# Performance work log

Measured on AMD Instinct MI355X. Metric: run time of the kernel, lower is better.

Reference implementation:

```python
import jax, jax.numpy as jnp
import numpy as np

LN_EPS = 1e-12


def setup_inputs() -> dict:
    key = jax.random.key(0)
    ks = jax.random.split(key, 10)
    B, S, W, D, H = 16, 512, 5, 200, 768
    std = 0.02
    return {
        "layer_output": jax.random.normal(ks[0], (B, S, H), dtype=jnp.float32),
        "word_embeddings": jax.random.normal(ks[1], (B, S, W, D), dtype=jnp.float32),
        "word_mask": jax.random.randint(ks[2], (B, S, W), 0, 2, dtype=jnp.int64),
        "W1": jax.random.normal(ks[3], (D, H), dtype=jnp.float32) * std,
        "b1": jnp.zeros((H,), dtype=jnp.float32),
        "W2": jax.random.normal(ks[4], (H, H), dtype=jnp.float32) * std,
        "b2": jnp.zeros((H,), dtype=jnp.float32),
        "attn_W": jax.random.normal(ks[5], (H, H), dtype=jnp.float32) * std,
        "ln_gamma": jnp.ones((H,), dtype=jnp.float32),
        "ln_beta": jnp.zeros((H,), dtype=jnp.float32),
    }


def reference(layer_output, word_embeddings, word_mask, W1, b1, W2, b2, attn_W, ln_gamma, ln_beta):
    # word_transform: Linear -> Tanh -> Linear (dropout = identity in eval)
    we = jnp.tanh(jnp.einsum("bswd,dh->bswh", word_embeddings, W1) + b1)
    we = jnp.einsum("bswh,hk->bswk", we, W2) + b2  # [B,S,W,H]

    # bilinear word attention: (x @ attn_W) . word_outputs -> score over W
    q = jnp.einsum("bsh,hk->bsk", layer_output, attn_W)  # [B,S,H]
    alpha = jnp.einsum("bsk,bswk->bsw", q, we)            # [B,S,W]
    alpha = alpha + (1.0 - word_mask.astype(alpha.dtype)) * -10000.0
    alpha = jax.nn.softmax(alpha, axis=-1)

    # weighted sum over words + residual
    agg = jnp.einsum("bsw,bswh->bsh", alpha, we)
    h = layer_output + agg

    # LayerNorm (fuse_layer; dropout = identity in eval)
    mu = jnp.mean(h, axis=-1, keepdims=True)
    var = jnp.mean(jnp.square(h - mu), axis=-1, keepdims=True)
    return (h - mu) * jax.lax.rsqrt(var + LN_EPS) * ln_gamma + ln_beta
```

## Files before the change

### kernel.cpp

```cpp
#include <hip/hip_runtime.h>
#include <hip/hip_bf16.h>
#include <math.h>


typedef __attribute__((ext_vector_type(8))) short bf16x8;
typedef __attribute__((ext_vector_type(4))) float f32x4;

__device__ __forceinline__ unsigned short f2bf_bits(float f) {
    __hip_bfloat16 h = __float2bfloat16(f);
    return *reinterpret_cast<unsigned short*>(&h);
}
__device__ __forceinline__ float bf_bits2f(unsigned short u) {
    union { unsigned int i; float f; } v; v.i = ((unsigned int)u) << 16; return v.f;
}
__device__ __forceinline__ float tanh_fast(float x) {
    float xc = fminf(fmaxf(x, -9.f), 9.f);
    float t  = __expf(2.f * xc);
    return (t - 1.f) * __builtin_amdgcn_rcpf(t + 1.f);
}

__device__ __forceinline__ void async_cp16(const void* g, void* lds) {
#if __has_builtin(__builtin_amdgcn_global_load_lds)
    auto gp = (const __attribute__((address_space(1))) unsigned int*)g;
    auto lp = (__attribute__((address_space(3))) unsigned int*)lds;
    __builtin_amdgcn_global_load_lds(gp, lp, 16, 0, 0);
#else
    *(uint4*)lds = *(const uint4*)g;
#endif
}

__device__ __forceinline__ void sched_fence()  { asm volatile("" ::: "memory"); }
__device__ __forceinline__ void wait8_barrier(){ asm volatile("s_waitcnt vmcnt(8)\ns_barrier" ::: "memory"); }
__device__ __forceinline__ void wait0_barrier(){ asm volatile("s_waitcnt vmcnt(0)\ns_barrier" ::: "memory"); }
__device__ __forceinline__ void barrier_only() { asm volatile("s_barrier" ::: "memory"); }

template<bool HAS_BIAS, bool TANH_ACT, bool RESID, bool OUT_BF16, int N, int K, int KREAL>
__device__ __forceinline__ void gemm_body(
    const __hip_bfloat16* __restrict__ A,
    const __hip_bfloat16* __restrict__ Bt,
    const float* __restrict__ bias,
    const float* __restrict__ resid,
    void* __restrict__ outp,
    int m0, int n0, unsigned char* smem)
{
    constexpr int NIT = K / 64;

    const int tid  = threadIdx.x;
    const int lane = tid & 63;
    const int wave = tid >> 6;
    const int wm   = wave & 1;
    const int wn   = wave >> 1;

    const int rsub = lane >> 3;
    const int slot = lane & 7;
    const int kc   = slot ^ rsub;
    const __hip_bfloat16* gA = A  + (size_t)(m0 + wave * 32 + rsub) * K + kc * 8;
    const __hip_bfloat16* gB = Bt + (size_t)(n0 + wave * 32 + rsub) * K + kc * 8;
    unsigned short* lA0 = (unsigned short*)smem + wave * 2048 + lane * 8;
    unsigned short* lB0 = lA0 + 8192;

    const int row16 = lane & 15;
    const int kq    = lane >> 4;

    f32x4 acc[4][4];
#pragma unroll
    for (int i = 0; i < 4; i++)
#pragma unroll
        for (int j = 0; j < 4; j++) acc[i][j] = (f32x4){0.f, 0.f, 0.f, 0.f};

    auto stage = [&](int t) {
        unsigned short* lA = lA0 + (t & 1) * 16384;
        unsigned short* lB = lB0 + (t & 1) * 16384;
        const __hip_bfloat16* a = gA + t * 64;
        const __hip_bfloat16* b = gB + t * 64;
#pragma unroll
        for (int i = 0; i < 4; i++) {
            async_cp16(a + (size_t)(8 * i) * K, lA + i * 512);
            async_cp16(b + (size_t)(8 * i) * K, lB + i * 512);
        }
        sched_fence();
    };

    stage(0);
    if (NIT > 1) stage(1);

#pragma unroll
    for (int t = 0; t < NIT; ++t) {
        if (t == NIT - 1) wait0_barrier(); else wait8_barrier();

        const unsigned short* As = (const unsigned short*)(smem + (t & 1) * 32768);
        const unsigned short* Bs = As + 8192;
        const bool full = (t * 64 + 32 < KREAL);

        bf16x8 af[2][4], bg[2][4];
#pragma unroll
        for (int mi = 0; mi < 4; mi++) {
            const int r = wm * 64 + mi * 16 + row16;
            af[0][mi] = *(const bf16x8*)&As[r * 64 + (kq ^ (r & 7)) * 8];
            if (full) af[1][mi] = *(const bf16x8*)&As[r * 64 + ((4 + kq) ^ (r & 7)) * 8];
        }
#pragma unroll
        for (int ni = 0; ni < 4; ni++) {
            const int r = wn * 64 + ni * 16 + row16;
            bg[0][ni] = *(const bf16x8*)&Bs[r * 64 + (kq ^ (r & 7)) * 8];
            if (full) bg[1][ni] = *(const bf16x8*)&Bs[r * 64 + ((4 + kq) ^ (r & 7)) * 8];
        }
#pragma unroll
        for (int mi = 0; mi < 4; mi++)
#pragma unroll
            for (int ni = 0; ni < 4; ni++)
                acc[mi][ni] = __builtin_amdgcn_mfma_f32_16x16x32_bf16(
                    af[0][mi], bg[0][ni], acc[mi][ni], 0, 0, 0);
        if (full) {
#pragma unroll
            for (int mi = 0; mi < 4; mi++)
#pragma unroll
                for (int ni = 0; ni < 4; ni++)
                    acc[mi][ni] = __builtin_amdgcn_mfma_f32_16x16x32_bf16(
                        af[1][mi], bg[1][ni], acc[mi][ni], 0, 0, 0);
        }
        barrier_only();
        if (t + 2 < NIT) stage(t + 2);
    }

    if (OUT_BF16) {
        unsigned short* rep = (unsigned short*)smem;
#pragma unroll
        for (int ni = 0; ni < 4; ni++) {
            const int c = wn * 64 + ni * 16 + row16;
            float bcol = HAS_BIAS ? bias[n0 + c] : 0.f;
#pragma unroll
            for (int mi = 0; mi < 4; mi++)
#pragma unroll
                for (int r = 0; r < 4; r++) {
                    const int rr = wm * 64 + mi * 16 + kq * 4 + r;
                    float v = acc[mi][ni][r];
                    if (HAS_BIAS) v += bcol;
                    if (TANH_ACT) v = tanh_fast(v);
                    rep[rr * 132 + c] = f2bf_bits(v);
                }
        }
        __syncthreads();
#pragma unroll
        for (int p = 0; p < 8; p++) {
            const int lin = p * 256 + tid;
            const int row = lin >> 4;
            const int c8  = lin & 15;
            const unsigned short* s = &rep[row * 132 + c8 * 8];
            union { uint4 u; unsigned long long q[2]; } d;
            d.q[0] = *(const unsigned long long*)(s);
            d.q[1] = *(const unsigned long long*)(s + 4);
            *(uint4*)((__hip_bfloat16*)outp + (size_t)(m0 + row) * N + n0 + c8 * 8) = d.u;
        }
    } else {
        float* rep = (float*)smem;
#pragma unroll
        for (int h = 0; h < 2; h++) {
            if (wm == h) {
#pragma unroll
                for (int ni = 0; ni < 4; ni++) {
                    const int c = wn * 64 + ni * 16 + row16;
                    float bcol = HAS_BIAS ? bias[n0 + c] : 0.f;
#pragma unroll
                    for (int mi = 0; mi < 4; mi++)
#pragma unroll
                        for (int r = 0; r < 4; r++) {
                            const int rr = mi * 16 + kq * 4 + r;
                            float v = acc[mi][ni][r];
                            if (HAS_BIAS) v += bcol;
                            if (TANH_ACT) v = tanh_fast(v);
                            rep[rr * 132 + c] = v;
                        }
                }
            }
            __syncthreads();
#pragma unroll
            for (int p = 0; p < 8; p++) {
                const int lin = p * 256 + tid;
                const int row = lin >> 5;
                const int c4  = lin & 31;
                float4 v = *(const float4*)&rep[row * 132 + c4 * 4];
                const int grow = m0 + h * 64 + row;
                if (RESID) {
                    float4 rv = *(const float4*)&resid[(size_t)grow * N + n0 + c4 * 4];
                    v.x += rv.x; v.y += rv.y; v.z += rv.z; v.w += rv.w;
                }
                *(float4*)((float*)outp + (size_t)grow * N + n0 + c4 * 4) = v;
            }
            __syncthreads();
        }
    }
}

template<bool HAS_BIAS, bool TANH_ACT, bool RESID, bool OUT_BF16, int N, int K, int GX>
__global__ __launch_bounds__(256) void mfma_gemm(
    const __hip_bfloat16* __restrict__ A,
    const __hip_bfloat16* __restrict__ Bt,
    const float* __restrict__ bias,
    const float* __restrict__ resid,
    void* __restrict__ outp)
{
    __shared__ __align__(16) unsigned char smem[65536];
    int bx, by;
    {
        const int total = gridDim.x;
        const int per_xcd = total >> 3;
        if ((total & 7) == 0 && (per_xcd % GX) == 0) {
            int xcd = blockIdx.x & 7, idx = blockIdx.x >> 3;
            int lin = xcd * per_xcd + idx;
            by = lin / GX; bx = lin % GX;
        } else { by = blockIdx.x / GX; bx = blockIdx.x % GX; }
    }
    gemm_body<HAS_BIAS, TANH_ACT, RESID, OUT_BF16, N, K, K>(
        A, Bt, bias, resid, outp, by * 128, bx * 128, smem);
}

__global__ __launch_bounds__(256) void tct_kernel(
    const __hip_bfloat16* __restrict__ Eb,   const __hip_bfloat16* __restrict__ W1Tb,
    const float* __restrict__ b1,            __hip_bfloat16* __restrict__ Tb,
    const __hip_bfloat16* __restrict__ W2b,  const __hip_bfloat16* __restrict__ attnb,
    __hip_bfloat16* __restrict__ Ctb)
{
    __shared__ __align__(16) unsigned char smem[65536];
    if (blockIdx.x < 36) {
        const int id = blockIdx.x;
        gemm_body<false, false, false, true, 768, 768, 768>(
            W2b, attnb, nullptr, nullptr, Ctb, (id / 6) * 128, (id % 6) * 128, smem);
    } else {
        const int idq = blockIdx.x - 36;
        const int xcd = idq & 7, idx = idq >> 3;
        const int lin = xcd * 240 + idx;
        gemm_body<true, true, false, true, 768, 256, 224>(
            Eb, W1Tb, b1, nullptr, Tb, (lin / 6) * 128, (lin % 6) * 128, smem);
    }
}

__global__ __launch_bounds__(256) void prep_kernel(
    const float* __restrict__ x,  __hip_bfloat16* __restrict__ xb,
    const float* __restrict__ w2, __hip_bfloat16* __restrict__ w2b,
    const float* __restrict__ aw, __hip_bfloat16* __restrict__ awb,
    const float* __restrict__ E,  __hip_bfloat16* __restrict__ Eb,
    const float* __restrict__ W1, __hip_bfloat16* __restrict__ W1Tb,
    __hip_bfloat16* __restrict__ W2Tb)
{
    __shared__ float tile[32][33];
    const int b = blockIdx.x, tid = threadIdx.x;
    if (b < 6144 + 576 + 576) {
        const float* src; __hip_bfloat16* dst; long long i;
        if (b < 6144)      { src = x;  dst = xb;  i = (long long)b * 256 + tid; }
        else if (b < 6720) { src = w2; dst = w2b; i = (long long)(b - 6144) * 256 + tid; }
        else               { src = aw; dst = awb; i = (long long)(b - 6720) * 256 + tid; }
        float4 v = ((const float4*)src)[i];
        ((ushort4*)dst)[i] = make_ushort4(f2bf_bits(v.x), f2bf_bits(v.y), f2bf_bits(v.z), f2bf_bits(v.w));
    } else if (b < 7296 + 10240) {
        const int lane = tid & 63, wave = tid >> 6;
        const long long row = (long long)(b - 7296) * 4 + wave;
        const int k = lane * 4;
        float4 v = make_float4(0.f, 0.f, 0.f, 0.f);
        if (k < 200) v = *(const float4*)&E[row * 200 + k];
        *(ushort4*)&Eb[row * 256 + k] =
            make_ushort4(f2bf_bits(v.x), f2bf_bits(v.y), f2bf_bits(v.z), f2bf_bits(v.w));
    } else {
        const float* in; __hip_bfloat16* outb; int R, C, Rpad, t;
        if (b < 17536 + 192) { t = b - 17536; in = W1; outb = W1Tb; R = 200; C = 768; Rpad = 256; }
        else                 { t = b - 17728; in = w2; outb = W2Tb; R = 768; C = 768; Rpad = 768; }
        const int c0 = (t % 24) * 32, r0 = (t / 24) * 32;
        const int xx = tid & 31, yy = tid >> 5;
#pragma unroll
        for (int i = 0; i < 32; i += 8) {
            int r = r0 + yy + i;
            tile[yy + i][xx] = (r < R) ? in[(size_t)r * C + c0 + xx] : 0.f;
        }
        __syncthreads();
#pragma unroll
        for (int i = 0; i < 32; i += 8)
            outb[(size_t)(c0 + yy + i) * Rpad + r0 + xx] = __float2bfloat16(tile[xx][yy + i]);
    }
}

__global__ __launch_bounds__(256) void attn_kernel(
    const __hip_bfloat16* __restrict__ T,
    const __hip_bfloat16* P,
    const int* __restrict__ mask,
    __hip_bfloat16* S)
{
    const int lane = threadIdx.x & 63;
    const int wave = threadIdx.x >> 6;
    const int r    = blockIdx.x * 4 + wave;
    const int base = lane * 12;

    float pv[12];
    {
        const ushort4* pp = (const ushort4*)((const unsigned short*)P + (size_t)r * 768 + base);
        ushort4 u0 = pp[0], u1 = pp[1], u2 = pp[2];
        unsigned short us[12] = {u0.x,u0.y,u0.z,u0.w, u1.x,u1.y,u1.z,u1.w, u2.x,u2.y,u2.z,u2.w};
#pragma unroll
        for (int j = 0; j < 12; j++) pv[j] = bf_bits2f(us[j]);
    }
    float tv[5][12], part[5];
#pragma unroll
    for (int w = 0; w < 5; w++) {
        const ushort4* tp = (const ushort4*)((const unsigned short*)T + ((size_t)r * 5 + w) * 768 + base);
        ushort4 u0 = tp[0], u1 = tp[1], u2 = tp[2];
        unsigned short us[12] = {u0.x,u0.y,u0.z,u0.w, u1.x,u1.y,u1.z,u1.w, u2.x,u2.y,u2.z,u2.w};
        float s = 0.f;
#pragma unroll
        for (int j = 0; j < 12; j++) { tv[w][j] = bf_bits2f(us[j]); s += tv[w][j] * pv[j]; }
        part[w] = s;
    }
#pragma unroll
    for (int off = 32; off > 0; off >>= 1)
#pragma unroll
        for (int w = 0; w < 5; w++)
            part[w] += __shfl_xor(part[w], off, 64);

    float logit[5], mx = -1e30f;
#pragma unroll
    for (int w = 0; w < 5; w++) {
        float m = (float)mask[(size_t)r * 5 + w];
        logit[w] = part[w] - 10000.0f * (1.0f - m);
        mx = fmaxf(mx, logit[w]);
    }
    float se = 0.f;
#pragma unroll
    for (int w = 0; w < 5; w++) { logit[w] = expf(logit[w] - mx); se += logit[w]; }
    const float inv = 1.0f / se;

    unsigned short os[12];
#pragma unroll
    for (int j = 0; j < 12; j++) {
        float s = 0.f;
#pragma unroll
        for (int w = 0; w < 5; w++) s += logit[w] * tv[w][j];
        os[j] = f2bf_bits(s * inv);
    }
    ushort4* sp = (ushort4*)((unsigned short*)S + (size_t)r * 768 + base);
    sp[0] = make_ushort4(os[0], os[1], os[2],  os[3]);
    sp[1] = make_ushort4(os[4], os[5], os[6],  os[7]);
    sp[2] = make_ushort4(os[8], os[9], os[10], os[11]);
}

__global__ __launch_bounds__(256) void ln_kernel(
    const float* __restrict__ Hbuf, const float* __restrict__ gamma,
    const float* __restrict__ beta, float* __restrict__ out)
{
    const int lane = threadIdx.x & 63;
    const int wave = threadIdx.x >> 6;
    const int r    = blockIdx.x * 4 + wave;
    const float* hr = Hbuf + (size_t)r * 768 + lane * 12;

    float v[12];
    {
        float4 a = *(const float4*)(hr);
        float4 b = *(const float4*)(hr + 4);
        float4 c = *(const float4*)(hr + 8);
        v[0]=a.x; v[1]=a.y; v[2]=a.z; v[3]=a.w;
        v[4]=b.x; v[5]=b.y; v[6]=b.z; v[7]=b.w;
        v[8]=c.x; v[9]=c.y; v[10]=c.z; v[11]=c.w;
    }
    float s = 0.f;
#pragma unroll
    for (int j = 0; j < 12; j++) s += v[j];
#pragma unroll
    for (int off = 32; off > 0; off >>= 1) s += __shfl_xor(s, off, 64);
    const float mu = s * (1.f / 768.f);
    float vs = 0.f;
#pragma unroll
    for (int j = 0; j < 12; j++) { float d = v[j] - mu; vs += d * d; }
#pragma unroll
    for (int off = 32; off > 0; off >>= 1) vs += __shfl_xor(vs, off, 64);
    const float rs = rsqrtf(vs * (1.f / 768.f) + 1e-12f);

    float o[12];
#pragma unroll
    for (int j = 0; j < 12; j++) {
        int h = lane * 12 + j;
        o[j] = (v[j] - mu) * rs * gamma[h] + beta[h];
    }
    float* orow = out + (size_t)r * 768 + lane * 12;
    *(float4*)(orow)     = make_float4(o[0], o[1], o[2],  o[3]);
    *(float4*)(orow + 4) = make_float4(o[4], o[5], o[6],  o[7]);
    *(float4*)(orow + 8) = make_float4(o[8], o[9], o[10], o[11]);
}

extern "C" void kernel_launch(void* const* d_in, const int* in_sizes, int n_in,
                              void* d_out, int out_size, void* d_ws, size_t ws_size,
                              hipStream_t stream)
{
    const float* x      = (const float*)d_in[0];
    const float* E      = (const float*)d_in[1];
    const int*   mask   = (const int*)d_in[2];
    const float* W1     = (const float*)d_in[3];
    const float* b1     = (const float*)d_in[4];
    const float* W2     = (const float*)d_in[5];
    const float* b2     = (const float*)d_in[6];
    const float* attn_W = (const float*)d_in[7];
    const float* gamma  = (const float*)d_in[8];
    const float* beta   = (const float*)d_in[9];
    float* out = (float*)d_out;

    const int BS = 8192, H = 768, M1 = 40960, KP = 256;

    char* p = (char*)d_ws;
    auto alloc = [&](size_t bytes) { char* q = p; p += (bytes + 255) & ~(size_t)255; return q; };
    __hip_bfloat16* xb    = (__hip_bfloat16*)alloc((size_t)BS * H * 2);
    __hip_bfloat16* W2b   = (__hip_bfloat16*)alloc((size_t)H * H * 2);
    __hip_bfloat16* W2Tb  = (__hip_bfloat16*)alloc((size_t)H * H * 2);
    __hip_bfloat16* attnb = (__hip_bfloat16*)alloc((size_t)H * H * 2);
    __hip_bfloat16* Ctb   = (__hip_bfloat16*)alloc((size_t)H * H * 2);
    __hip_bfloat16* W1Tb  = (__hip_bfloat16*)alloc((size_t)H * KP * 2);
    __hip_bfloat16* Tb    = (__hip_bfloat16*)alloc((size_t)M1 * H * 2);
    __hip_bfloat16* Eb    = (__hip_bfloat16*)alloc((size_t)M1 * KP * 2);
    float* Hb = (float*)Tb;
    __hip_bfloat16* Pb = Eb;
    __hip_bfloat16* Sb = Pb;

    prep_kernel<<<18304, 256, 0, stream>>>(x, xb, W2, W2b, attn_W, attnb,
                                           E, Eb, W1, W1Tb, W2Tb);

    tct_kernel<<<1956, 256, 0, stream>>>(Eb, W1Tb, b1, Tb, W2b, attnb, Ctb);

    mfma_gemm<false, false, false, true, 768, 768, 6><<<384, 256, 0, stream>>>(
        xb, Ctb, nullptr, nullptr, Pb);
    attn_kernel<<<BS / 4, 256, 0, stream>>>(Tb, Pb, mask, Sb);
    mfma_gemm<true, false, true, false, 768, 768, 6><<<384, 256, 0, stream>>>(
        Sb, W2Tb, b2, x, Hb);
    ln_kernel<<<BS / 4, 256, 0, stream>>>(Hb, gamma, beta, out);
}
```

Measured before the change: 211.8 us.

## Fuse word-transform GEMM with attention softmax and fold weight product into prep

Merges the E@W1+tanh GEMM with the bilinear attention/softmax/weighted-sum step into one kernel. Each block keeps its 60 rows of tanh output (12 positions × 5 words) in LDS instead of writing the large T intermediate to global memory and reading it back. The W2·attn_W product is now computed inside the prep kernel straight from fp32 sources, removing the separate bf16 conversions and the tct launch. The cost is a very large LDS footprint per block (about 148 KB), which limits occupancy to one block per CU. It also uses a smaller M tile, so W1 tiles are reloaded more often and GEMM efficiency may drop.

Measured after the change: 247.1 us. +16.7%, slower.

```diff
diff --git a/kernel.cpp b/kernel.cpp
--- a/kernel.cpp
+++ b/kernel.cpp
@@ -17,6 +17,12 @@
     float xc = fminf(fmaxf(x, -9.f), 9.f);
     float t  = __expf(2.f * xc);
     return (t - 1.f) * __builtin_amdgcn_rcpf(t + 1.f);
+}
+__device__ __forceinline__ bf16x8 pack8(float4 a, float4 b) {
+    union { bf16x8 v; unsigned short s[8]; } u;
+    u.s[0]=f2bf_bits(a.x); u.s[1]=f2bf_bits(a.y); u.s[2]=f2bf_bits(a.z); u.s[3]=f2bf_bits(a.w);
+    u.s[4]=f2bf_bits(b.x); u.s[5]=f2bf_bits(b.y); u.s[6]=f2bf_bits(b.z); u.s[7]=f2bf_bits(b.w);
+    return u.v;
 }
 
 __device__ __forceinline__ void async_cp16(const void* g, void* lds) {
@@ -31,34 +37,22 @@
 
 __device__ __forceinline__ void sched_fence()  { asm volatile("" ::: "memory"); }
 __device__ __forceinline__ void wait8_barrier(){ asm volatile("s_waitcnt vmcnt(8)\ns_barrier" ::: "memory"); }
+__device__ __forceinline__ void wait6_barrier(){ asm volatile("s_waitcnt vmcnt(6)\ns_barrier" ::: "memory"); }
 __device__ __forceinline__ void wait0_barrier(){ asm volatile("s_waitcnt vmcnt(0)\ns_barrier" ::: "memory"); }
 __device__ __forceinline__ void barrier_only() { asm volatile("s_barrier" ::: "memory"); }
 
-template<bool HAS_BIAS, bool TANH_ACT, bool RESID, bool OUT_BF16, int N, int K, int KREAL>
+template<bool F32SRC, bool HAS_BIAS, bool TANH_ACT, bool RESID, bool OUT_BF16, int N, int K, int KREAL>
 __device__ __forceinline__ void gemm_body(
-    const __hip_bfloat16* __restrict__ A,
-    const __hip_bfloat16* __restrict__ Bt,
-    const float* __restrict__ bias,
-    const float* __restrict__ resid,
-    void* __restrict__ outp,
-    int m0, int n0, unsigned char* smem)
+    const void* __restrict__ Ap, const void* __restrict__ Btp,
+    const float* __restrict__ bias, const float* __restrict__ resid,
+    void* __restrict__ outp, int m0, int n0, unsigned char* smem)
 {
     constexpr int NIT = K / 64;
-
     const int tid  = threadIdx.x;
     const int lane = tid & 63;
     const int wave = tid >> 6;
     const int wm   = wave & 1;
     const int wn   = wave >> 1;
-
-    const int rsub = lane >> 3;
-    const int slot = lane & 7;
-    const int kc   = slot ^ rsub;
-    const __hip_bfloat16* gA = A  + (size_t)(m0 + wave * 32 + rsub) * K + kc * 8;
-    const __hip_bfloat16* gB = Bt + (size_t)(n0 + wave * 32 + rsub) * K + kc * 8;
-    unsigned short* lA0 = (unsigned short*)smem + wave * 2048 + lane * 8;
-    unsigned short* lB0 = lA0 + 8192;
-
     const int row16 = lane & 15;
     const int kq    = lane >> 4;
 
@@ -68,30 +62,7 @@
 #pragma unroll
         for (int j = 0; j < 4; j++) acc[i][j] = (f32x4){0.f, 0.f, 0.f, 0.f};
 
-    auto stage = [&](int t) {
-        unsigned short* lA = lA0 + (t & 1) * 16384;
-        unsigned short* lB = lB0 + (t & 1) * 16384;
-        const __hip_bfloat16* a = gA + t * 64;
-        const __hip_bfloat16* b = gB + t * 64;
-#pragma unroll
-        for (int i = 0; i < 4; i++) {
-            async_cp16(a + (size_t)(8 * i) * K, lA + i * 512);
-            async_cp16(b + (size_t)(8 * i) * K, lB + i * 512);
-        }
-        sched_fence();
-    };
-
-    stage(0);
-    if (NIT > 1) stage(1);
-
-#pragma unroll
-    for (int t = 0; t < NIT; ++t) {
-        if (t == NIT - 1) wait0_barrier(); else wait8_barrier();
-
-        const unsigned short* As = (const unsigned short*)(smem + (t & 1) * 32768);
-        const unsigned short* Bs = As + 8192;
-        const bool full = (t * 64 + 32 < KREAL);
-
+    auto compute_tile = [&](const unsigned short* As, const unsigned short* Bs, bool full) {
         bf16x8 af[2][4], bg[2][4];
 #pragma unroll
         for (int mi = 0; mi < 4; mi++) {
@@ -105,6 +76,7 @@
             bg[0][ni] = *(const bf16x8*)&Bs[r * 64 + (kq ^ (r & 7)) * 8];
             if (full) bg[1][ni] = *(const bf16x8*)&Bs[r * 64 + ((4 + kq) ^ (r & 7)) * 8];
         }
+        __builtin_amdgcn_s_setprio(1);
 #pragma unroll
         for (int mi = 0; mi < 4; mi++)
 #pragma unroll
@@ -119,8 +91,64 @@
                     acc[mi][ni] = __builtin_amdgcn_mfma_f32_16x16x32_bf16(
                         af[1][mi], bg[1][ni], acc[mi][ni], 0, 0, 0);
         }
-        barrier_only();
-        if (t + 2 < NIT) stage(t + 2);
+        __builtin_amdgcn_s_setprio(0);
+    };
+
+    if constexpr (F32SRC) {
+        const float* A32 = (const float*)Ap;
+        const float* B32 = (const float*)Btp;
+        unsigned short* As = (unsigned short*)smem;
+        unsigned short* Bs = As + 8192;
+        for (int t = 0; t < NIT; ++t) {
+#pragma unroll
+            for (int i = 0; i < 4; ++i) {
+                const int c = i * 256 + tid;
+                const int row = c >> 3, sl = c & 7;
+                const int kcc = sl ^ (row & 7);
+                const float* sa = A32 + (size_t)(m0 + row) * K + t * 64 + kcc * 8;
+                *(bf16x8*)&As[row * 64 + sl * 8] = pack8(*(const float4*)sa, *(const float4*)(sa + 4));
+                const float* sb = B32 + (size_t)(n0 + row) * K + t * 64 + kcc * 8;
+                *(bf16x8*)&Bs[row * 64 + sl * 8] = pack8(*(const float4*)sb, *(const float4*)(sb + 4));
+            }
+            __syncthreads();
+            compute_tile(As, Bs, true);
+            __syncthreads();
+        }
+    } else {
+        const __hip_bfloat16* A  = (const __hip_bfloat16*)Ap;
+        const __hip_bfloat16* Bt = (const __hip_bfloat16*)Btp;
+        const int rsub = lane >> 3;
+        const int slot = lane & 7;
+        const int kc   = slot ^ rsub;
+        const __hip_bfloat16* gA = A  + (size_t)(m0 + wave * 32 + rsub) * K + kc * 8;
+        const __hip_bfloat16* gB = Bt + (size_t)(n0 + wave * 32 + rsub) * K + kc * 8;
+        unsigned short* lA0 = (unsigned short*)smem + wave * 2048 + lane * 8;
+        unsigned short* lB0 = lA0 + 8192;
+
+        auto stage = [&](int t) {
+            unsigned short* lA = lA0 + (t & 1) * 16384;
+            unsigned short* lB = lB0 + (t & 1) * 16384;
+            const __hip_bfloat16* a = gA + t * 64;
+            const __hip_bfloat16* b = gB + t * 64;
+#pragma unroll
+            for (int i = 0; i < 4; i++) {
+                async_cp16(a + (size_t)(8 * i) * K, lA + i * 512);
+                async_cp16(b + (size_t)(8 * i) * K, lB + i * 512);
+            }
+            sched_fence();
+        };
+
+        stage(0);
+        if (NIT > 1) stage(1);
+#pragma unroll
+        for (int t = 0; t < NIT; ++t) {
+            if (t == NIT - 1) wait0_barrier(); else wait8_barrier();
+            const unsigned short* As = (const unsigned short*)(smem + (t & 1) * 32768);
+            const unsigned short* Bs = As + 8192;
+            compute_tile(As, Bs, (t * 64 + 32 < KREAL));
+            barrier_only();
+            if (t + 2 < NIT) stage(t + 2);
+        }
     }
 
     if (OUT_BF16) {
@@ -211,59 +239,209 @@
             by = lin / GX; bx = lin % GX;
         } else { by = blockIdx.x / GX; bx = blockIdx.x % GX; }
     }
-    gemm_body<HAS_BIAS, TANH_ACT, RESID, OUT_BF16, N, K, K>(
+    gemm_body<false, HAS_BIAS, TANH_ACT, RESID, OUT_BF16, N, K, K>(
         A, Bt, bias, resid, outp, by * 128, bx * 128, smem);
 }
 
-__global__ __launch_bounds__(256) void tct_kernel(
-    const __hip_bfloat16* __restrict__ Eb,   const __hip_bfloat16* __restrict__ W1Tb,
-    const float* __restrict__ b1,            __hip_bfloat16* __restrict__ Tb,
-    const __hip_bfloat16* __restrict__ W2b,  const __hip_bfloat16* __restrict__ attnb,
+__global__ __launch_bounds__(256) void tatt_kernel(
+    const __hip_bfloat16* __restrict__ Eb,
+    const __hip_bfloat16* __restrict__ W1Tb,
+    const float* __restrict__ b1,
+    const __hip_bfloat16* __restrict__ P,
+    const int* __restrict__ mask,
+    __hip_bfloat16* __restrict__ S)
+{
+    __shared__ __align__(16) unsigned char smem[147968];
+    unsigned short* Tl = (unsigned short*)smem;
+    unsigned char*  stg = smem + 98816;
+
+    const int tid  = threadIdx.x;
+    const int lane = tid & 63;
+    const int wave = tid >> 6;
+    const int wm   = wave & 1;
+    const int wn   = wave >> 1;
+    const int row16 = lane & 15;
+    const int kq    = lane >> 4;
+    const int m0   = blockIdx.x * 60;
+
+    auto stage = [&](int nt_, int kt_, int buf) {
+        unsigned short* lA = (unsigned short*)(stg + buf * 24576);
+        unsigned short* lB = lA + 4096;
+#pragma unroll
+        for (int i = 0; i < 2; i++) {
+            const int c = i * 256 + wave * 64 + lane;
+            const int row = c >> 3, sl = c & 7;
+            const int kcc = sl ^ (row & 7);
+            async_cp16(Eb + (size_t)(m0 + row) * 256 + kt_ * 64 + kcc * 8, lA + c * 8);
+        }
+#pragma unroll
+        for (int i = 0; i < 4; i++) {
+            const int c = i * 256 + wave * 64 + lane;
+            const int row = c >> 3, sl = c & 7;
+            const int kcc = sl ^ (row & 7);
+            async_cp16(W1Tb + (size_t)(nt_ * 128 + row) * 256 + kt_ * 64 + kcc * 8, lB + c * 8);
+        }
+        sched_fence();
+    };
+
+    stage(0, 0, 0);
+    stage(0, 1, 1);
+
+    for (int nt = 0; nt < 6; ++nt) {
+        f32x4 acc[2][4];
+#pragma unroll
+        for (int i = 0; i < 2; i++)
+#pragma unroll
+            for (int j = 0; j < 4; j++) acc[i][j] = (f32x4){0.f, 0.f, 0.f, 0.f};
+
+#pragma unroll
+        for (int kt = 0; kt < 4; ++kt) {
+            wait6_barrier();
+            const unsigned short* As = (const unsigned short*)(stg + (kt & 1) * 24576);
+            const unsigned short* Bs = As + 4096;
+            const bool full = (kt < 3);
+
+            bf16x8 af[2][2], bg[2][4];
+#pragma unroll
+            for (int mi = 0; mi < 2; mi++) {
+                const int r = wm * 32 + mi * 16 + row16;
+                af[0][mi] = *(const bf16x8*)&As[r * 64 + (kq ^ (r & 7)) * 8];
+                if (full) af[1][mi] = *(const bf16x8*)&As[r * 64 + ((4 + kq) ^ (r & 7)) * 8];
+            }
+#pragma unroll
+            for (int ni = 0; ni < 4; ni++) {
+                const int r = wn * 64 + ni * 16 + row16;
+                bg[0][ni] = *(const bf16x8*)&Bs[r * 64 + (kq ^ (r & 7)) * 8];
+                if (full) bg[1][ni] = *(const bf16x8*)&Bs[r * 64 + ((4 + kq) ^ (r & 7)) * 8];
+            }
+            __builtin_amdgcn_s_setprio(1);
+#pragma unroll
+            for (int mi = 0; mi < 2; mi++)
+#pragma unroll
+                for (int ni = 0; ni < 4; ni++)
+                    acc[mi][ni] = __builtin_amdgcn_mfma_f32_16x16x32_bf16(
+                        af[0][mi], bg[0][ni], acc[mi][ni], 0, 0, 0);
+            if (full) {
+#pragma unroll
+                for (int mi = 0; mi < 2; mi++)
+#pragma unroll
+                    for (int ni = 0; ni < 4; ni++)
+                        acc[mi][ni] = __builtin_amdgcn_mfma_f32_16x16x32_bf16(
+                            af[1][mi], bg[1][ni], acc[mi][ni], 0, 0, 0);
+            }
+            __builtin_amdgcn_s_setprio(0);
+            barrier_only();
+            {
+                const int kt2 = (kt + 2) & 3;
+                int nt2 = nt + (kt >= 2 ? 1 : 0);
+                if (nt2 > 5) nt2 = 5;
+                stage(nt2, kt2, kt2 & 1);
+            }
+        }
+
+#pragma unroll
+        for (int ni = 0; ni < 4; ni++) {
+            const int c = wn * 64 + ni * 16 + row16;
+            const float bcol = b1[nt * 128 + c];
+#pragma unroll
+            for (int mi = 0; mi < 2; mi++)
+#pragma unroll
+                for (int r = 0; r < 4; r++) {
+                    const int rr = wm * 32 + mi * 16 + kq * 4 + r;
+                    Tl[rr * 772 + nt * 128 + c] = f2bf_bits(tanh_fast(acc[mi][ni][r] + bcol));
+                }
+        }
+    }
+    __syncthreads();
+
+    const int g0 = blockIdx.x * 12;
+    const int base = lane * 12;
+#pragma unroll
+    for (int t = 0; t < 3; ++t) {
+        const int j  = wave * 3 + t;
+        const int gg = g0 + j;
+        if (gg < 8192) {
+            float pv[12];
+            {
+                const ushort4* pp = (const ushort4*)((const unsigned short*)P + (size_t)gg * 768 + base);
+                ushort4 u0 = pp[0], u1 = pp[1], u2 = pp[2];
+                unsigned short us[12] = {u0.x,u0.y,u0.z,u0.w, u1.x,u1.y,u1.z,u1.w, u2.x,u2.y,u2.z,u2.w};
+#pragma unroll
+                for (int q = 0; q < 12; q++) pv[q] = bf_bits2f(us[q]);
+            }
+            float tv[5][12], part[5];
+#pragma unroll
+            for (int w = 0; w < 5; w++) {
+                const ushort4* tp = (const ushort4*)&Tl[(size_t)(j * 5 + w) * 772 + base];
+                ushort4 u0 = tp[0], u1 = tp[1], u2 = tp[2];
+                unsigned short us[12] = {u0.x,u0.y,u0.z,u0.w, u1.x,u1.y,u1.z,u1.w, u2.x,u2.y,u2.z,u2.w};
+                float s = 0.f;
+#pragma unroll
+                for (int q = 0; q < 12; q++) { tv[w][q] = bf_bits2f(us[q]); s += tv[w][q] * pv[q]; }
+                part[w] = s;
+            }
+#pragma unroll
+            for (int off = 32; off > 0; off >>= 1)
+#pragma unroll
+                for (int w = 0; w < 5; w++)
+                    part[w] += __shfl_xor(part[w], off, 64);
+
+            float logit[5], mx = -1e30f;
+#pragma unroll
+            for (int w = 0; w < 5; w++) {
+                float m = (float)mask[(size_t)gg * 5 + w];
+                logit[w] = part[w] - 10000.0f * (1.0f - m);
+                mx = fmaxf(mx, logit[w]);
+            }
+            float se = 0.f;
+#pragma unroll
+            for (int w = 0; w < 5; w++) { logit[w] = expf(logit[w] - mx); se += logit[w]; }
+            const float inv = 1.0f / se;
+
+            unsigned short os[12];
+#pragma unroll
+            for (int q = 0; q < 12; q++) {
+                float s = 0.f;
+#pragma unroll
+                for (int w = 0; w < 5; w++) s += logit[w] * tv[w][q];
+                os[q] = f2bf_bits(s * inv);
+            }
+            ushort4* sp = (ushort4*)((unsigned short*)S + (size_t)gg * 768 + base);
+            sp[0] = make_ushort4(os[0], os[1], os[2],  os[3]);
+            sp[1] = make_ushort4(os[4], os[5], os[6],  os[7]);
+            sp[2] = make_ushort4(os[8], os[9], os[10], os[11]);
+        }
+    }
+}
+
+__global__ __launch_bounds__(256) void prep_kernel(
+    const float* __restrict__ x,  __hip_bfloat16* __restrict__ xb,
+    const float* __restrict__ w2,
+    const float* __restrict__ aw,
+    const float* __restrict__ E,  __hip_bfloat16* __restrict__ Eb,
+    const float* __restrict__ W1, __hip_bfloat16* __restrict__ W1Tb,
+    __hip_bfloat16* __restrict__ W2Tb,
     __hip_bfloat16* __restrict__ Ctb)
 {
-    __shared__ __align__(16) unsigned char smem[65536];
-    if (blockIdx.x < 36) {
-        const int id = blockIdx.x;
-        gemm_body<false, false, false, true, 768, 768, 768>(
-            W2b, attnb, nullptr, nullptr, Ctb, (id / 6) * 128, (id % 6) * 128, smem);
-    } else {
-        const int idq = blockIdx.x - 36;
-        const int xcd = idq & 7, idx = idq >> 3;
-        const int lin = xcd * 240 + idx;
-        gemm_body<true, true, false, true, 768, 256, 224>(
-            Eb, W1Tb, b1, nullptr, Tb, (lin / 6) * 128, (lin % 6) * 128, smem);
-    }
-}
-
-__global__ __launch_bounds__(256) void prep_kernel(
-    const float* __restrict__ x,  __hip_bfloat16* __restrict__ xb,
-    const float* __restrict__ w2, __hip_bfloat16* __restrict__ w2b,
-    const float* __restrict__ aw, __hip_bfloat16* __restrict__ awb,
-    const float* __restrict__ E,  __hip_bfloat16* __restrict__ Eb,
-    const float* __restrict__ W1, __hip_bfloat16* __restrict__ W1Tb,
-    __hip_bfloat16* __restrict__ W2Tb)
-{
-    __shared__ float tile[32][33];
+    __shared__ __align__(16) unsigned char smem[33792];
+    float (*tile)[33] = (float(*)[33])smem;
     const int b = blockIdx.x, tid = threadIdx.x;
-    if (b < 6144 + 576 + 576) {
-        const float* src; __hip_bfloat16* dst; long long i;
-        if (b < 6144)      { src = x;  dst = xb;  i = (long long)b * 256 + tid; }
-        else if (b < 6720) { src = w2; dst = w2b; i = (long long)(b - 6144) * 256 + tid; }
-        else               { src = aw; dst = awb; i = (long long)(b - 6720) * 256 + tid; }
-        float4 v = ((const float4*)src)[i];
-        ((ushort4*)dst)[i] = make_ushort4(f2bf_bits(v.x), f2bf_bits(v.y), f2bf_bits(v.z), f2bf_bits(v.w));
-    } else if (b < 7296 + 10240) {
+    if (b < 6144) {
+        long long i = (long long)b * 256 + tid;
+        float4 v = ((const float4*)x)[i];
+        ((ushort4*)xb)[i] = make_ushort4(f2bf_bits(v.x), f2bf_bits(v.y), f2bf_bits(v.z), f2bf_bits(v.w));
+    } else if (b < 16384) {
         const int lane = tid & 63, wave = tid >> 6;
-        const long long row = (long long)(b - 7296) * 4 + wave;
+        const long long row = (long long)(b - 6144) * 4 + wave;
         const int k = lane * 4;
         float4 v = make_float4(0.f, 0.f, 0.f, 0.f);
         if (k < 200) v = *(const float4*)&E[row * 200 + k];
         *(ushort4*)&Eb[row * 256 + k] =
             make_ushort4(f2bf_bits(v.x), f2bf_bits(v.y), f2bf_bits(v.z), f2bf_bits(v.w));
-    } else {
+    } else if (b < 17152) {
         const float* in; __hip_bfloat16* outb; int R, C, Rpad, t;
-        if (b < 17536 + 192) { t = b - 17536; in = W1; outb = W1Tb; R = 200; C = 768; Rpad = 256; }
-        else                 { t = b - 17728; in = w2; outb = W2Tb; R = 768; C = 768; Rpad = 768; }
+        if (b < 16576) { t = b - 16384; in = W1; outb = W1Tb; R = 200; C = 768; Rpad = 256; }
+        else           { t = b - 16576; in = w2; outb = W2Tb; R = 768; C = 768; Rpad = 768; }
         const int c0 = (t % 24) * 32, r0 = (t / 24) * 32;
         const int xx = tid & 31, yy = tid >> 5;
 #pragma unroll
@@ -275,69 +453,11 @@
 #pragma unroll
         for (int i = 0; i < 32; i += 8)
             outb[(size_t)(c0 + yy + i) * Rpad + r0 + xx] = __float2bfloat16(tile[xx][yy + i]);
-    }
-}
-
-__global__ __launch_bounds__(256) void attn_kernel(
-    const __hip_bfloat16* __restrict__ T,
-    const __hip_bfloat16* P,
-    const int* __restrict__ mask,
-    __hip_bfloat16* S)
-{
-    const int lane = threadIdx.x & 63;
-    const int wave = threadIdx.x >> 6;
-    const int r    = blockIdx.x * 4 + wave;
-    const int base = lane * 12;
-
-    float pv[12];
-    {
-        const ushort4* pp = (const ushort4*)((const unsigned short*)P + (size_t)r * 768 + base);
-        ushort4 u0 = pp[0], u1 = pp[1], u2 = pp[2];
-        unsigned short us[12] = {u0.x,u0.y,u0.z,u0.w, u1.x,u1.y,u1.z,u1.w, u2.x,u2.y,u2.z,u2.w};
-#pragma unroll
-        for (int j = 0; j < 12; j++) pv[j] = bf_bits2f(us[j]);
-    }
-    float tv[5][12], part[5];
-#pragma unroll
-    for (int w = 0; w < 5; w++) {
-        const ushort4* tp = (const ushort4*)((const unsigned short*)T + ((size_t)r * 5 + w) * 768 + base);
-        ushort4 u0 = tp[0], u1 = tp[1], u2 = tp[2];
-        unsigned short us[12] = {u0.x,u0.y,u0.z,u0.w, u1.x,u1.y,u1.z,u1.w, u2.x,u2.y,u2.z,u2.w};
-        float s = 0.f;
-#pragma unroll
-        for (int j = 0; j < 12; j++) { tv[w][j] = bf_bits2f(us[j]); s += tv[w][j] * pv[j]; }
-        part[w] = s;
-    }
-#pragma unroll
-    for (int off = 32; off > 0; off >>= 1)
-#pragma unroll
-        for (int w = 0; w < 5; w++)
-            part[w] += __shfl_xor(part[w], off, 64);
-
-    float logit[5], mx = -1e30f;
-#pragma unroll
-    for (int w = 0; w < 5; w++) {
-        float m = (float)mask[(size_t)r * 5 + w];
-        logit[w] = part[w] - 10000.0f * (1.0f - m);
-        mx = fmaxf(mx, logit[w]);
-    }
-    float se = 0.f;
-#pragma unroll
-    for (int w = 0; w < 5; w++) { logit[w] = expf(logit[w] - mx); se += logit[w]; }
-    const float inv = 1.0f / se;
-
-    unsigned short os[12];
-#pragma unroll
-    for (int j = 0; j < 12; j++) {
-        float s = 0.f;
-#pragma unroll
-        for (int w = 0; w < 5; w++) s += logit[w] * tv[w][j];
-        os[j] = f2bf_bits(s * inv);
-    }
-    ushort4* sp = (ushort4*)((unsigned short*)S + (size_t)r * 768 + base);
-    sp[0] = make_ushort4(os[0], os[1], os[2],  os[3]);
-    sp[1] = make_ushort4(os[4], os[5], os[6],  os[7]);
-    sp[2] = make_ushort4(os[8], os[9], os[10], os[11]);
+    } else {
+        const int id = b - 17152;
+        gemm_body<true, false, false, false, true, 768, 768, 768>(
+            w2, aw, nullptr, nullptr, Ctb, (id / 6) * 128, (id % 6) * 128, smem);
+    }
 }
 
 __global__ __launch_bounds__(256) void ln_kernel(
@@ -404,26 +524,23 @@
     char* p = (char*)d_ws;
     auto alloc = [&](size_t bytes) { char* q = p; p += (bytes + 255) & ~(size_t)255; return q; };
     __hip_bfloat16* xb    = (__hip_bfloat16*)alloc((size_t)BS * H * 2);
-    __hip_bfloat16* W2b   = (__hip_bfloat16*)alloc((size_t)H * H * 2);
     __hip_bfloat16* W2Tb  = (__hip_bfloat16*)alloc((size_t)H * H * 2);
-    __hip_bfloat16* attnb = (__hip_bfloat16*)alloc((size_t)H * H * 2);
     __hip_bfloat16* Ctb   = (__hip_bfloat16*)alloc((size_t)H * H * 2);
     __hip_bfloat16* W1Tb  = (__hip_bfloat16*)alloc((size_t)H * KP * 2);
-    __hip_bfloat16* Tb    = (__hip_bfloat16*)alloc((size_t)M1 * H * 2);
-    __hip_bfloat16* Eb    = (__hip_bfloat16*)alloc((size_t)M1 * KP * 2);
-    float* Hb = (float*)Tb;
-    __hip_bfloat16* Pb = Eb;
-    __hip_bfloat16* Sb = Pb;
-
-    prep_kernel<<<18304, 256, 0, stream>>>(x, xb, W2, W2b, attn_W, attnb,
-                                           E, Eb, W1, W1Tb, W2Tb);
-
-    tct_kernel<<<1956, 256, 0, stream>>>(Eb, W1Tb, b1, Tb, W2b, attnb, Ctb);
+    __hip_bfloat16* Eb    = (__hip_bfloat16*)alloc((size_t)(M1 + 64) * KP * 2);
+    __hip_bfloat16* Pb    = (__hip_bfloat16*)alloc((size_t)BS * H * 2);
+    float*          Hb    = (float*)alloc((size_t)BS * H * 4);
+    __hip_bfloat16* Sb    = Pb;
+
+    prep_kernel<<<17188, 256, 0, stream>>>(x, xb, W2, attn_W, E, Eb, W1, W1Tb, W2Tb, Ctb);
 
     mfma_gemm<false, false, false, true, 768, 768, 6><<<384, 256, 0, stream>>>(
         xb, Ctb, nullptr, nullptr, Pb);
-    attn_kernel<<<BS / 4, 256, 0, stream>>>(Tb, Pb, mask, Sb);
+
+    tatt_kernel<<<683, 256, 0, stream>>>(Eb, W1Tb, b1, Pb, mask, Sb);
+
     mfma_gemm<true, false, true, false, 768, 768, 6><<<384, 256, 0, stream>>>(
         Sb, W2Tb, b2, x, Hb);
+
     ln_kernel<<<BS / 4, 256, 0, stream>>>(Hb, gamma, beta, out);
 }
```

## Move W2·attnᵀ GEMM into prep kernel and single-stage-load the T GEMM

Applied to the files above, without the earlier changes.

The small 768x768 W2·attn product is now computed in the prep kernel straight from fp32 inputs, converting to bf16 on the fly while staging into LDS. This drops the separate W2/attn bf16 conversion passes and their buffers. The E·W1 GEMM moves to its own kernel that loads the whole K=256 slab into 128KB of LDS at once instead of double-buffering. MFMA sections are also wrapped in s_setprio. The catch is the large LDS footprint, which lowers occupancy for the T GEMM, and a long serial GEMM tail inside prep blocks that may not overlap well.

Result: slower. 252.0 us (+19.0%).

```diff
diff --git a/kernel.cpp b/kernel.cpp
--- a/kernel.cpp
+++ b/kernel.cpp
@@ -17,6 +17,12 @@
     float xc = fminf(fmaxf(x, -9.f), 9.f);
     float t  = __expf(2.f * xc);
     return (t - 1.f) * __builtin_amdgcn_rcpf(t + 1.f);
+}
+__device__ __forceinline__ bf16x8 pack8(float4 a, float4 b) {
+    union { bf16x8 v; unsigned short s[8]; } u;
+    u.s[0]=f2bf_bits(a.x); u.s[1]=f2bf_bits(a.y); u.s[2]=f2bf_bits(a.z); u.s[3]=f2bf_bits(a.w);
+    u.s[4]=f2bf_bits(b.x); u.s[5]=f2bf_bits(b.y); u.s[6]=f2bf_bits(b.z); u.s[7]=f2bf_bits(b.w);
+    return u.v;
 }
 
 __device__ __forceinline__ void async_cp16(const void* g, void* lds) {
@@ -34,31 +40,19 @@
 __device__ __forceinline__ void wait0_barrier(){ asm volatile("s_waitcnt vmcnt(0)\ns_barrier" ::: "memory"); }
 __device__ __forceinline__ void barrier_only() { asm volatile("s_barrier" ::: "memory"); }
 
-template<bool HAS_BIAS, bool TANH_ACT, bool RESID, bool OUT_BF16, int N, int K, int KREAL>
+template<bool F32SRC, bool SINGLE, bool HAS_BIAS, bool TANH_ACT, bool RESID, bool OUT_BF16,
+         int N, int K, int KREAL>
 __device__ __forceinline__ void gemm_body(
-    const __hip_bfloat16* __restrict__ A,
-    const __hip_bfloat16* __restrict__ Bt,
-    const float* __restrict__ bias,
-    const float* __restrict__ resid,
-    void* __restrict__ outp,
-    int m0, int n0, unsigned char* smem)
+    const void* __restrict__ Ap, const void* __restrict__ Btp,
+    const float* __restrict__ bias, const float* __restrict__ resid,
+    void* __restrict__ outp, int m0, int n0, unsigned char* smem)
 {
     constexpr int NIT = K / 64;
-
     const int tid  = threadIdx.x;
     const int lane = tid & 63;
     const int wave = tid >> 6;
     const int wm   = wave & 1;
     const int wn   = wave >> 1;
-
-    const int rsub = lane >> 3;
-    const int slot = lane & 7;
-    const int kc   = slot ^ rsub;
-    const __hip_bfloat16* gA = A  + (size_t)(m0 + wave * 32 + rsub) * K + kc * 8;
-    const __hip_bfloat16* gB = Bt + (size_t)(n0 + wave * 32 + rsub) * K + kc * 8;
-    unsigned short* lA0 = (unsigned short*)smem + wave * 2048 + lane * 8;
-    unsigned short* lB0 = lA0 + 8192;
-
     const int row16 = lane & 15;
     const int kq    = lane >> 4;
 
@@ -68,30 +62,7 @@
 #pragma unroll
         for (int j = 0; j < 4; j++) acc[i][j] = (f32x4){0.f, 0.f, 0.f, 0.f};
 
-    auto stage = [&](int t) {
-        unsigned short* lA = lA0 + (t & 1) * 16384;
-        unsigned short* lB = lB0 + (t & 1) * 16384;
-        const __hip_bfloat16* a = gA + t * 64;
-        const __hip_bfloat16* b = gB + t * 64;
-#pragma unroll
-        for (int i = 0; i < 4; i++) {
-            async_cp16(a + (size_t)(8 * i) * K, lA + i * 512);
-            async_cp16(b + (size_t)(8 * i) * K, lB + i * 512);
-        }
-        sched_fence();
-    };
-
-    stage(0);
-    if (NIT > 1) stage(1);
-
-#pragma unroll
-    for (int t = 0; t < NIT; ++t) {
-        if (t == NIT - 1) wait0_barrier(); else wait8_barrier();
-
-        const unsigned short* As = (const unsigned short*)(smem + (t & 1) * 32768);
-        const unsigned short* Bs = As + 8192;
-        const bool full = (t * 64 + 32 < KREAL);
-
+    auto compute_tile = [&](const unsigned short* As, const unsigned short* Bs, bool full) {
         bf16x8 af[2][4], bg[2][4];
 #pragma unroll
         for (int mi = 0; mi < 4; mi++) {
@@ -105,6 +76,7 @@
             bg[0][ni] = *(const bf16x8*)&Bs[r * 64 + (kq ^ (r & 7)) * 8];
             if (full) bg[1][ni] = *(const bf16x8*)&Bs[r * 64 + ((4 + kq) ^ (r & 7)) * 8];
         }
+        __builtin_amdgcn_s_setprio(1);
 #pragma unroll
         for (int mi = 0; mi < 4; mi++)
 #pragma unroll
@@ -119,8 +91,77 @@
                     acc[mi][ni] = __builtin_amdgcn_mfma_f32_16x16x32_bf16(
                         af[1][mi], bg[1][ni], acc[mi][ni], 0, 0, 0);
         }
-        barrier_only();
-        if (t + 2 < NIT) stage(t + 2);
+        __builtin_amdgcn_s_setprio(0);
+    };
+
+    if constexpr (F32SRC) {
+        const float* A32 = (const float*)Ap;
+        const float* B32 = (const float*)Btp;
+        unsigned short* As = (unsigned short*)smem;
+        unsigned short* Bs = As + 8192;
+        for (int t = 0; t < NIT; ++t) {
+#pragma unroll
+            for (int i = 0; i < 4; ++i) {
+                const int c = i * 256 + tid;
+                const int row = c >> 3, sl = c & 7;
+                const int kcc = sl ^ (row & 7);
+                const float* sa = A32 + (size_t)(m0 + row) * K + t * 64 + kcc * 8;
+                *(bf16x8*)&As[row * 64 + sl * 8] = pack8(*(const float4*)sa, *(const float4*)(sa + 4));
+                const float* sb = B32 + (size_t)(n0 + row) * K + t * 64 + kcc * 8;
+                *(bf16x8*)&Bs[row * 64 + sl * 8] = pack8(*(const float4*)sb, *(const float4*)(sb + 4));
+            }
+            __syncthreads();
+            compute_tile(As, Bs, true);
+            __syncthreads();
+        }
+    } else {
+        const __hip_bfloat16* A  = (const __hip_bfloat16*)Ap;
+        const __hip_bfloat16* Bt = (const __hip_bfloat16*)Btp;
+        const int rsub = lane >> 3;
+        const int slot = lane & 7;
+        const int kc   = slot ^ rsub;
+        const __hip_bfloat16* gA = A  + (size_t)(m0 + wave * 32 + rsub) * K + kc * 8;
+        const __hip_bfloat16* gB = Bt + (size_t)(n0 + wave * 32 + rsub) * K + kc * 8;
+        unsigned short* lA0 = (unsigned short*)smem + wave * 2048 + lane * 8;
+        unsigned short* lB0 = lA0 + 8192;
+
+        auto stage = [&](int t, int buf) {
+            unsigned short* lA = lA0 + buf * 16384;
+            unsigned short* lB = lB0 + buf * 16384;
+            const __hip_bfloat16* a = gA + t * 64;
+            const __hip_bfloat16* b = gB + t * 64;
+#pragma unroll
+            for (int i = 0; i < 4; i++) {
+                async_cp16(a + (size_t)(8 * i) * K, lA + i * 512);
+                async_cp16(b + (size_t)(8 * i) * K, lB + i * 512);
+            }
+            sched_fence();
+        };
+
+        if constexpr (SINGLE) {
+            static_assert(!SINGLE || NIT <= 4, "SINGLE path needs K<=256 (128KB LDS)");
+#pragma unroll
+            for (int t = 0; t < NIT; ++t) stage(t, t);
+            wait0_barrier();
+#pragma unroll
+            for (int t = 0; t < NIT; ++t) {
+                const unsigned short* As = (const unsigned short*)(smem + t * 32768);
+                compute_tile(As, As + 8192, (t * 64 + 32 < KREAL));
+            }
+            barrier_only();
+        } else {
+            stage(0, 0);
+            if (NIT > 1) stage(1, 1);
+#pragma unroll
+            for (int t = 0; t < NIT; ++t) {
+                if (t == NIT - 1) wait0_barrier(); else wait8_barrier();
+                const unsigned short* As = (const unsigned short*)(smem + (t & 1) * 32768);
+                const unsigned short* Bs = As + 8192;
+                compute_tile(As, Bs, (t * 64 + 32 < KREAL));
+                barrier_only();
+                if (t + 2 < NIT) stage(t + 2, t & 1);
+            }
+        }
     }
 
     if (OUT_BF16) {
@@ -211,59 +252,51 @@
             by = lin / GX; bx = lin % GX;
         } else { by = blockIdx.x / GX; bx = blockIdx.x % GX; }
     }
-    gemm_body<HAS_BIAS, TANH_ACT, RESID, OUT_BF16, N, K, K>(
+    gemm_body<false, false, HAS_BIAS, TANH_ACT, RESID, OUT_BF16, N, K, K>(
         A, Bt, bias, resid, outp, by * 128, bx * 128, smem);
 }
 
-__global__ __launch_bounds__(256) void tct_kernel(
-    const __hip_bfloat16* __restrict__ Eb,   const __hip_bfloat16* __restrict__ W1Tb,
-    const float* __restrict__ b1,            __hip_bfloat16* __restrict__ Tb,
-    const __hip_bfloat16* __restrict__ W2b,  const __hip_bfloat16* __restrict__ attnb,
-    __hip_bfloat16* __restrict__ Ctb)
-{
-    __shared__ __align__(16) unsigned char smem[65536];
-    if (blockIdx.x < 36) {
-        const int id = blockIdx.x;
-        gemm_body<false, false, false, true, 768, 768, 768>(
-            W2b, attnb, nullptr, nullptr, Ctb, (id / 6) * 128, (id % 6) * 128, smem);
-    } else {
-        const int idq = blockIdx.x - 36;
-        const int xcd = idq & 7, idx = idq >> 3;
-        const int lin = xcd * 240 + idx;
-        gemm_body<true, true, false, true, 768, 256, 224>(
-            Eb, W1Tb, b1, nullptr, Tb, (lin / 6) * 128, (lin % 6) * 128, smem);
-    }
+__global__ __launch_bounds__(256) void tgemm_kernel(
+    const __hip_bfloat16* __restrict__ Eb,
+    const __hip_bfloat16* __restrict__ W1Tb,
+    const float* __restrict__ b1,
+    __hip_bfloat16* __restrict__ Tb)
+{
+    __shared__ __align__(16) unsigned char smem[131072];
+    const int xcd = blockIdx.x & 7, idx = blockIdx.x >> 3;
+    const int lin = xcd * 240 + idx;
+    gemm_body<false, true, true, true, false, true, 768, 256, 224>(
+        Eb, W1Tb, b1, nullptr, Tb, (lin / 6) * 128, (lin % 6) * 128, smem);
 }
 
 __global__ __launch_bounds__(256) void prep_kernel(
     const float* __restrict__ x,  __hip_bfloat16* __restrict__ xb,
-    const float* __restrict__ w2, __hip_bfloat16* __restrict__ w2b,
-    const float* __restrict__ aw, __hip_bfloat16* __restrict__ awb,
+    const float* __restrict__ w2,
+    const float* __restrict__ aw,
     const float* __restrict__ E,  __hip_bfloat16* __restrict__ Eb,
     const float* __restrict__ W1, __hip_bfloat16* __restrict__ W1Tb,
-    __hip_bfloat16* __restrict__ W2Tb)
-{
-    __shared__ float tile[32][33];
+    __hip_bfloat16* __restrict__ W2Tb,
+    __hip_bfloat16* __restrict__ Ctb)
+{
+    __shared__ __align__(16) unsigned char smem[33792];
+    float (*tile)[33] = (float(*)[33])smem;
     const int b = blockIdx.x, tid = threadIdx.x;
-    if (b < 6144 + 576 + 576) {
-        const float* src; __hip_bfloat16* dst; long long i;
-        if (b < 6144)      { src = x;  dst = xb;  i = (long long)b * 256 + tid; }
-        else if (b < 6720) { src = w2; dst = w2b; i = (long long)(b - 6144) * 256 + tid; }
-        else               { src = aw; dst = awb; i = (long long)(b - 6720) * 256 + tid; }
-        float4 v = ((const float4*)src)[i];
-        ((ushort4*)dst)[i] = make_ushort4(f2bf_bits(v.x), f2bf_bits(v.y), f2bf_bits(v.z), f2bf_bits(v.w));
-    } else if (b < 7296 + 10240) {
+    if (b < 6144) {
+        long long i = (long long)b * 256 + tid;
+        float4 v = ((const float4*)x)[i];
+        ((ushort4*)xb)[i] = make_ushort4(f2bf_bits(v.x), f2bf_bits(v.y), f2bf_bits(v.z), f2bf_bits(v.w));
+    } else if (b < 16384) {
         const int lane = tid & 63, wave = tid >> 6;
-        const long long row = (long long)(b - 7296) * 4 + wave;
+        const long long row = (long long)(b - 6144) * 4 + wave;
         const int k = lane * 4;
         float4 v = make_float4(0.f, 0.f, 0.f, 0.f);
         if (k < 200) v = *(const float4*)&E[row * 200 + k];
         *(ushort4*)&Eb[row * 256 + k] =
             make_ushort4(f2bf_bits(v.x), f2bf_bits(v.y), f2bf_bits(v.z), f2bf_bits(v.w));
-    } else {
+    } else if (b < 17152) {
         const float* in; __hip_bfloat16* outb; int R, C, Rpad, t;
-        if (b < 17536 + 192) { t = b - 17536; in = W1; outb = W1Tb; R = 200; C = 768; Rpad = 256; }
-        else                 { t = b - 17728; in = w2; outb = W2Tb; R = 768; C = 768; Rpad = 768; }
+        if (b < 16576) { t = b - 16384; in = W1; outb = W1Tb; R = 200; C = 768; Rpad = 256; }
+        else           { t = b - 16576; in = w2; outb = W2Tb; R = 768; C = 768; Rpad = 768; }
         const int c0 = (t % 24) * 32, r0 = (t / 24) * 32;
         const int xx = tid & 31, yy = tid >> 5;
 #pragma unroll
@@ -275,6 +308,10 @@
 #pragma unroll
         for (int i = 0; i < 32; i += 8)
             outb[(size_t)(c0 + yy + i) * Rpad + r0 + xx] = __float2bfloat16(tile[xx][yy + i]);
+    } else {
+        const int id = b - 17152;
+        gemm_body<true, false, false, false, false, true, 768, 768, 768>(
+            w2, aw, nullptr, nullptr, Ctb, (id / 6) * 128, (id % 6) * 128, smem);
     }
 }
 
@@ -404,9 +441,7 @@
     char* p = (char*)d_ws;
     auto alloc = [&](size_t bytes) { char* q = p; p += (bytes + 255) & ~(size_t)255; return q; };
     __hip_bfloat16* xb    = (__hip_bfloat16*)alloc((size_t)BS * H * 2);
-    __hip_bfloat16* W2b   = (__hip_bfloat16*)alloc((size_t)H * H * 2);
     __hip_bfloat16* W2Tb  = (__hip_bfloat16*)alloc((size_t)H * H * 2);
-    __hip_bfloat16* attnb = (__hip_bfloat16*)alloc((size_t)H * H * 2);
     __hip_bfloat16* Ctb   = (__hip_bfloat16*)alloc((size_t)H * H * 2);
     __hip_bfloat16* W1Tb  = (__hip_bfloat16*)alloc((size_t)H * KP * 2);
     __hip_bfloat16* Tb    = (__hip_bfloat16*)alloc((size_t)M1 * H * 2);
@@ -415,15 +450,17 @@
     __hip_bfloat16* Pb = Eb;
     __hip_bfloat16* Sb = Pb;
 
-    prep_kernel<<<18304, 256, 0, stream>>>(x, xb, W2, W2b, attn_W, attnb,
-                                           E, Eb, W1, W1Tb, W2Tb);
-
-    tct_kernel<<<1956, 256, 0, stream>>>(Eb, W1Tb, b1, Tb, W2b, attnb, Ctb);
+    prep_kernel<<<17188, 256, 0, stream>>>(x, xb, W2, attn_W, E, Eb, W1, W1Tb, W2Tb, Ctb);
+
+    tgemm_kernel<<<1920, 256, 0, stream>>>(Eb, W1Tb, b1, Tb);
 
     mfma_gemm<false, false, false, true, 768, 768, 6><<<384, 256, 0, stream>>>(
         xb, Ctb, nullptr, nullptr, Pb);
+
     attn_kernel<<<BS / 4, 256, 0, stream>>>(Tb, Pb, mask, Sb);
+
     mfma_gemm<true, false, true, false, 768, 768, 6><<<384, 256, 0, stream>>>(
         Sb, W2Tb, b2, x, Hb);
+
     ln_kernel<<<BS / 4, 256, 0, stream>>>(Hb, gamma, beta, out);
 }
```
